# Kernel tuning notes

Hardware: AMD Instinct MI355X
Metric: run time of the kernel (lower is better)

The kernel has to match this reference:

```python
import jax, jax.numpy as jnp
from jax import lax
import numpy as np


def setup_inputs() -> dict:
    key = jax.random.key(0)
    ks = jax.random.split(key, 7)
    B, T, F, H, O = 4096, 256, 18, 64, 15
    s = 1.0 / np.sqrt(H)  # PyTorch uniform(-1/sqrt(H), 1/sqrt(H)) init scale
    return {
        "X": jax.random.normal(ks[0], (B, T, F), dtype=jnp.float32),
        "W_ih": jax.random.uniform(ks[1], (4 * H, F), jnp.float32, -s, s),
        "W_hh": jax.random.uniform(ks[2], (4 * H, H), jnp.float32, -s, s),
        "b_ih": jax.random.uniform(ks[3], (4 * H,), jnp.float32, -s, s),
        "b_hh": jax.random.uniform(ks[4], (4 * H,), jnp.float32, -s, s),
        "W_cls": jax.random.uniform(ks[5], (O, H), jnp.float32, -s, s),
        "b_cls": jax.random.uniform(ks[6], (O,), jnp.float32, -s, s),
    }


def _lstm_last_h(X, W_ih, W_hh, b_ih, b_hh):
    # X: [B, T, F]; PyTorch gate order in the 4H axis: i, f, g, o
    B = X.shape[0]
    H = W_hh.shape[1]
    # Input contribution for all timesteps at once: [B, T, 4H]
    xg = jnp.einsum("btf,gf->btg", X, W_ih) + b_ih + b_hh
    xg_t = jnp.swapaxes(xg, 0, 1)  # [T, B, 4H] for scan over time

    def step(carry, xg_step):
        h, c = carry
        gates = xg_step + h @ W_hh.T  # [B, 4H]
        i, f, g, o = jnp.split(gates, 4, axis=-1)
        i = jax.nn.sigmoid(i)
        f = jax.nn.sigmoid(f)
        g = jnp.tanh(g)
        o = jax.nn.sigmoid(o)
        c = f * c + i * g
        h = o * jnp.tanh(c)
        return (h, c), None

    h0 = jnp.zeros((B, H), dtype=X.dtype)
    c0 = jnp.zeros((B, H), dtype=X.dtype)
    (h, c), _ = lax.scan(step, (h0, c0), xg_t)
    return h  # last-timestep hidden state, [B, H]


def reference(X, W_ih, W_hh, b_ih, b_hh, W_cls, b_cls):
    h_last = _lstm_last_h(X, W_ih, W_hh, b_ih, b_hh)
    out = h_last @ W_cls.T + b_cls  # [B, n_outputs]
    return out
```

## Files before the change

kernel.cpp:

```cpp
#include <hip/hip_runtime.h>
#include <hip/hip_bf16.h>

typedef __attribute__((ext_vector_type(8))) __bf16 bf16x8;
typedef __attribute__((ext_vector_type(4))) float  f32x4;

#define T_SEQ 256
#define F_IN  18
#define HID   64
#define NB    16
#define NO    15

static __device__ __forceinline__ float rcp_fast(float x) {
    return __builtin_amdgcn_rcpf(x);
}
static __device__ __forceinline__ float sigm(float x) {
    return rcp_fast(1.0f + __expf(-x));
}
static __device__ __forceinline__ float tanh_fast(float x) {
    return 1.0f - 2.0f * rcp_fast(__expf(2.0f * x) + 1.0f);
}

#define BARRIER_LDS() asm volatile("s_waitcnt lgkmcnt(0)\n\ts_barrier" ::: "memory")

__global__ __launch_bounds__(1024, 4) void lstm_fused(
    const float* __restrict__ X,
    const float* __restrict__ Wih,
    const float* __restrict__ Whh,
    const float* __restrict__ bih,
    const float* __restrict__ bhh,
    const float* __restrict__ Wcls,
    const float* __restrict__ bcls,
    float* __restrict__ out)
{
    const int tid = threadIdx.x;
    const int l   = tid & 63;
    const int w   = tid >> 6;
    const int q   = l >> 4;
    const int bb  = l & 15;
    const int b0  = blockIdx.x * NB;

    __shared__ __align__(16) __bf16 hbuf[2][2][8][NB][8];
    __shared__ __align__(16) __bf16 xbuf[2][8][NB][8];
    __shared__ float h32[NB][HID];

    const int sb = (tid >> 3) & 15;
    const int sk = ((tid >> 7) << 3) | (tid & 7);
    int f_s, part_s;
    if (sk < 18)      { f_s = sk;      part_s = 0; }
    else if (sk < 36) { f_s = sk - 18; part_s = 0; }
    else if (sk < 54) { f_s = sk - 36; part_s = 1; }
    else              { f_s = 0;       part_s = 2; }
    const float* xsrc = X + ((long)(b0 + sb) * T_SEQ) * F_IN + f_s;
    __bf16* const xbase = &xbuf[0][0][0][0];

    {
        __bf16* hz = &hbuf[0][0][0][0][0];
        for (int i = tid; i < 2 * 8 * NB * 8; i += 1024) hz[i] = (__bf16)0.0f;
    }
    {
        const float v = (part_s == 2) ? 0.0f : xsrc[0];
        const __bf16 hi = (__bf16)v;
        xbase[tid] = (part_s == 1) ? (__bf16)(v - (float)hi) : hi;
    }
    float xq[4];
#pragma unroll
    for (int i = 0; i < 4; ++i)
        xq[i] = (part_s == 2) ? 0.0f : xsrc[(1 + i) * F_IN];

    bf16x8 whh_hi[2], whh_lo[2], wih[2];
    {
        const int prow = 16 * w + bb;
        const int jrow = (prow & 3) * 64 + (prow >> 2);
#pragma unroll
        for (int kk = 0; kk < 2; ++kk) {
            bf16x8 hi, lo, xa;
#pragma unroll
            for (int r = 0; r < 8; ++r) {
                const int k = 32 * kk + 8 * q + r;
                const float v = Whh[jrow * HID + k];
                const __bf16 vh = (__bf16)v;
                hi[r] = vh;
                lo[r] = (__bf16)(v - (float)vh);
                int f, part;
                if (k < 18)      { f = k;      part = 0; }
                else if (k < 36) { f = k - 18; part = 1; }
                else if (k < 54) { f = k - 36; part = 0; }
                else             { f = 0;      part = 2; }
                const float wv = (part == 2) ? 0.0f : Wih[jrow * F_IN + f];
                const __bf16 wh = (__bf16)wv;
                xa[r] = (part == 1) ? (__bf16)(wv - (float)wh) : wh;
            }
            whh_hi[kk] = hi;
            whh_lo[kk] = lo;
            wih[kk]    = xa;
        }
    }

    const int u_c = 4 * w + q;
    float bias4[4];
#pragma unroll
    for (int r = 0; r < 4; ++r) bias4[r] = bih[r * 64 + u_c] + bhh[r * 64 + u_c];

    __bf16* const hw_base = &hbuf[0][0][0][0][0] +
                            ((u_c >> 3) * 128 + bb * 8 + (u_c & 7));
    const __bf16* const hr_base = &hbuf[0][0][0][0][0] + 8 * (size_t)l;
    const __bf16* const xr_base = &xbuf[0][0][0][0] + 8 * (size_t)l;

    __syncthreads();

    float cst = 0.0f;

#pragma unroll 4
    for (int t = 0; t < T_SEQ; ++t) {
        const int cur = t & 1;
        const int nxt = cur ^ 1;
        const int s   = t & 3;

        const __bf16* hr = hr_base + cur * 2048;
        const __bf16* xr = xr_base + cur * 1024;
        const bf16x8 bx0 = *reinterpret_cast<const bf16x8*>(xr);
        const bf16x8 bx1 = *reinterpret_cast<const bf16x8*>(xr + 512);
        const bf16x8 bh0 = *reinterpret_cast<const bf16x8*>(hr);
        const bf16x8 bh1 = *reinterpret_cast<const bf16x8*>(hr + 512);
        const bf16x8 bl0 = *reinterpret_cast<const bf16x8*>(hr + 1024);
        const bf16x8 bl1 = *reinterpret_cast<const bf16x8*>(hr + 1536);

        {
            const float vs = xq[s];
            const __bf16 sh = (__bf16)vs;
            xbase[nxt * 1024 + tid] = (part_s == 1) ? (__bf16)(vs - (float)sh) : sh;
        }
        {
            const int tload = (t + 5 < T_SEQ) ? (t + 5) : (T_SEQ - 1);
            xq[s] = (part_s == 2) ? 0.0f : xsrc[tload * F_IN];
        }

        f32x4 acc_a = {bias4[0], bias4[1], bias4[2], bias4[3]};
        f32x4 acc_b = {0.0f, 0.0f, 0.0f, 0.0f};
        f32x4 acc_c = {0.0f, 0.0f, 0.0f, 0.0f};
        f32x4 acc_d = {0.0f, 0.0f, 0.0f, 0.0f};
        acc_a = __builtin_amdgcn_mfma_f32_16x16x32_bf16(wih[0],    bx0, acc_a, 0, 0, 0);
        acc_b = __builtin_amdgcn_mfma_f32_16x16x32_bf16(wih[1],    bx1, acc_b, 0, 0, 0);
        acc_c = __builtin_amdgcn_mfma_f32_16x16x32_bf16(whh_lo[0], bh0, acc_c, 0, 0, 0);
        acc_d = __builtin_amdgcn_mfma_f32_16x16x32_bf16(whh_lo[1], bh1, acc_d, 0, 0, 0);
        acc_a = __builtin_amdgcn_mfma_f32_16x16x32_bf16(whh_hi[0], bh0, acc_a, 0, 0, 0);
        acc_b = __builtin_amdgcn_mfma_f32_16x16x32_bf16(whh_hi[1], bh1, acc_b, 0, 0, 0);
        acc_c = __builtin_amdgcn_mfma_f32_16x16x32_bf16(whh_hi[0], bl0, acc_c, 0, 0, 0);
        acc_d = __builtin_amdgcn_mfma_f32_16x16x32_bf16(whh_hi[1], bl1, acc_d, 0, 0, 0);

        const f32x4 acc = (acc_a + acc_b) + (acc_c + acc_d);

        const float gi = sigm(acc[0]);
        const float gf = sigm(acc[1]);
        const float gg = tanh_fast(acc[2]);
        const float go = sigm(acc[3]);
        const float c  = gf * cst + gi * gg;
        cst = c;
        const float h  = go * tanh_fast(c);
        const __bf16 hh = (__bf16)h;
        const __bf16 hl = (__bf16)(h - (float)hh);
        __bf16* hw = hw_base + nxt * 2048;
        hw[0]    = hh;
        hw[1024] = hl;
        if (t == T_SEQ - 1) h32[bb][u_c] = h;

        BARRIER_LDS();
    }

    if (tid < NB * NO) {
        const int bo = tid / NO;
        const int o  = tid % NO;
        float ssum = bcls[o];
#pragma unroll 8
        for (int k = 0; k < HID; ++k)
            ssum += h32[bo][k] * Wcls[o * HID + k];
        out[(long)(b0 + bo) * NO + o] = ssum;
    }
}

extern "C" void kernel_launch(void* const* d_in, const int* in_sizes, int n_in,
                              void* d_out, int out_size, void* d_ws, size_t ws_size,
                              hipStream_t stream)
{
    const float* X    = (const float*)d_in[0];
    const float* Wih  = (const float*)d_in[1];
    const float* Whh  = (const float*)d_in[2];
    const float* bih  = (const float*)d_in[3];
    const float* bhh  = (const float*)d_in[4];
    const float* Wcls = (const float*)d_in[5];
    const float* bcls = (const float*)d_in[6];
    float* outp = (float*)d_out;

    dim3 grid(4096 / NB);
    dim3 block(1024);
    lstm_fused<<<grid, block, 0, stream>>>(X, Wih, Whh, bih, bhh, Wcls, bcls, outp);
}
```

Measured before the change: 282.8 us.

## Drop bf16 low part of hidden state, peel loop tail, add MFMA priority

Stores the recurrent hidden state as a single bf16 value instead of a hi/lo pair. This halves the h LDS buffer and reads, and cuts the per-step MFMA count from eight to six. The main loop is split into a 248-step body without the prefetch clamp or last-step check, plus a fully unrolled tail. s_setprio is raised around the MFMA and activation section. The cost is lower precision in the recurrence: h is rounded to bf16 with no compensation term, which may push the output error past tolerance over 256 steps.

```diff
diff --git a/kernel.cpp b/kernel.cpp
--- a/kernel.cpp
+++ b/kernel.cpp
@@ -39,7 +39,7 @@
     const int bb  = l & 15;
     const int b0  = blockIdx.x * NB;
 
-    __shared__ __align__(16) __bf16 hbuf[2][2][8][NB][8];
+    __shared__ __align__(16) __bf16 hbuf[2][8][NB][8];
     __shared__ __align__(16) __bf16 xbuf[2][8][NB][8];
     __shared__ float h32[NB][HID];
 
@@ -54,8 +54,8 @@
     __bf16* const xbase = &xbuf[0][0][0][0];
 
     {
-        __bf16* hz = &hbuf[0][0][0][0][0];
-        for (int i = tid; i < 2 * 8 * NB * 8; i += 1024) hz[i] = (__bf16)0.0f;
+        __bf16* hz = &hbuf[0][0][0][0];
+        for (int i = tid; i < 8 * NB * 8; i += 1024) hz[i] = (__bf16)0.0f;
     }
     {
         const float v = (part_s == 2) ? 0.0f : xsrc[0];
@@ -101,71 +101,69 @@
 #pragma unroll
     for (int r = 0; r < 4; ++r) bias4[r] = bih[r * 64 + u_c] + bhh[r * 64 + u_c];
 
-    __bf16* const hw_base = &hbuf[0][0][0][0][0] +
+    __bf16* const hw_base = &hbuf[0][0][0][0] +
                             ((u_c >> 3) * 128 + bb * 8 + (u_c & 7));
-    const __bf16* const hr_base = &hbuf[0][0][0][0][0] + 8 * (size_t)l;
+    const __bf16* const hr_base = &hbuf[0][0][0][0] + 8 * (size_t)l;
     const __bf16* const xr_base = &xbuf[0][0][0][0] + 8 * (size_t)l;
 
     __syncthreads();
 
     float cst = 0.0f;
 
+#define STEP(t_, PF, LAST)                                                          \
+    {                                                                               \
+        const int cur_ = (t_) & 1;                                                  \
+        const int nxt_ = cur_ ^ 1;                                                  \
+        const int s_   = (t_) & 3;                                                  \
+        const __bf16* hr = hr_base + cur_ * 1024;                                   \
+        const __bf16* xr = xr_base + cur_ * 1024;                                   \
+        const bf16x8 bx0 = *reinterpret_cast<const bf16x8*>(xr);                    \
+        const bf16x8 bx1 = *reinterpret_cast<const bf16x8*>(xr + 512);              \
+        const bf16x8 bh0 = *reinterpret_cast<const bf16x8*>(hr);                    \
+        const bf16x8 bh1 = *reinterpret_cast<const bf16x8*>(hr + 512);              \
+        {                                                                           \
+            const float vs = xq[s_];                                                \
+            const __bf16 sh = (__bf16)vs;                                           \
+            xbase[nxt_ * 1024 + tid] = (part_s == 1) ? (__bf16)(vs - (float)sh) : sh; \
+        }                                                                           \
+        {                                                                           \
+            const int tl_ = PF ? (((t_) + 5 < T_SEQ) ? (t_) + 5 : (T_SEQ - 1))      \
+                               : ((t_) + 5);                                        \
+            xq[s_] = (part_s == 2) ? 0.0f : xsrc[tl_ * F_IN];                       \
+        }                                                                           \
+        __builtin_amdgcn_s_setprio(1);                                              \
+        f32x4 acc_a = {bias4[0], bias4[1], bias4[2], bias4[3]};                     \
+        f32x4 acc_b = {0.0f, 0.0f, 0.0f, 0.0f};                                     \
+        f32x4 acc_c = {0.0f, 0.0f, 0.0f, 0.0f};                                     \
+        acc_a = __builtin_amdgcn_mfma_f32_16x16x32_bf16(wih[0],    bx0, acc_a, 0, 0, 0); \
+        acc_b = __builtin_amdgcn_mfma_f32_16x16x32_bf16(wih[1],    bx1, acc_b, 0, 0, 0); \
+        acc_c = __builtin_amdgcn_mfma_f32_16x16x32_bf16(whh_lo[0], bh0, acc_c, 0, 0, 0); \
+        acc_a = __builtin_amdgcn_mfma_f32_16x16x32_bf16(whh_hi[0], bh0, acc_a, 0, 0, 0); \
+        acc_b = __builtin_amdgcn_mfma_f32_16x16x32_bf16(whh_hi[1], bh1, acc_b, 0, 0, 0); \
+        acc_c = __builtin_amdgcn_mfma_f32_16x16x32_bf16(whh_lo[1], bh1, acc_c, 0, 0, 0); \
+        const f32x4 acc = (acc_a + acc_b) + acc_c;                                  \
+        const float gi = sigm(acc[0]);                                              \
+        const float gf = sigm(acc[1]);                                              \
+        const float gg = tanh_fast(acc[2]);                                         \
+        const float go = sigm(acc[3]);                                              \
+        const float c  = gf * cst + gi * gg;                                        \
+        cst = c;                                                                    \
+        const float h  = go * tanh_fast(c);                                         \
+        hw_base[nxt_ * 1024] = (__bf16)h;                                           \
+        __builtin_amdgcn_s_setprio(0);                                              \
+        if (LAST) h32[bb][u_c] = h;                                                 \
+        BARRIER_LDS();                                                              \
+    }
+
 #pragma unroll 4
-    for (int t = 0; t < T_SEQ; ++t) {
-        const int cur = t & 1;
-        const int nxt = cur ^ 1;
-        const int s   = t & 3;
-
-        const __bf16* hr = hr_base + cur * 2048;
-        const __bf16* xr = xr_base + cur * 1024;
-        const bf16x8 bx0 = *reinterpret_cast<const bf16x8*>(xr);
-        const bf16x8 bx1 = *reinterpret_cast<const bf16x8*>(xr + 512);
-        const bf16x8 bh0 = *reinterpret_cast<const bf16x8*>(hr);
-        const bf16x8 bh1 = *reinterpret_cast<const bf16x8*>(hr + 512);
-        const bf16x8 bl0 = *reinterpret_cast<const bf16x8*>(hr + 1024);
-        const bf16x8 bl1 = *reinterpret_cast<const bf16x8*>(hr + 1536);
-
-        {
-            const float vs = xq[s];
-            const __bf16 sh = (__bf16)vs;
-            xbase[nxt * 1024 + tid] = (part_s == 1) ? (__bf16)(vs - (float)sh) : sh;
-        }
-        {
-            const int tload = (t + 5 < T_SEQ) ? (t + 5) : (T_SEQ - 1);
-            xq[s] = (part_s == 2) ? 0.0f : xsrc[tload * F_IN];
-        }
-
-        f32x4 acc_a = {bias4[0], bias4[1], bias4[2], bias4[3]};
-        f32x4 acc_b = {0.0f, 0.0f, 0.0f, 0.0f};
-        f32x4 acc_c = {0.0f, 0.0f, 0.0f, 0.0f};
-        f32x4 acc_d = {0.0f, 0.0f, 0.0f, 0.0f};
-        acc_a = __builtin_amdgcn_mfma_f32_16x16x32_bf16(wih[0],    bx0, acc_a, 0, 0, 0);
-        acc_b = __builtin_amdgcn_mfma_f32_16x16x32_bf16(wih[1],    bx1, acc_b, 0, 0, 0);
-        acc_c = __builtin_amdgcn_mfma_f32_16x16x32_bf16(whh_lo[0], bh0, acc_c, 0, 0, 0);
-        acc_d = __builtin_amdgcn_mfma_f32_16x16x32_bf16(whh_lo[1], bh1, acc_d, 0, 0, 0);
-        acc_a = __builtin_amdgcn_mfma_f32_16x16x32_bf16(whh_hi[0], bh0, acc_a, 0, 0, 0);
-        acc_b = __builtin_amdgcn_mfma_f32_16x16x32_bf16(whh_hi[1], bh1, acc_b, 0, 0, 0);
-        acc_c = __builtin_amdgcn_mfma_f32_16x16x32_bf16(whh_hi[0], bl0, acc_c, 0, 0, 0);
-        acc_d = __builtin_amdgcn_mfma_f32_16x16x32_bf16(whh_hi[1], bl1, acc_d, 0, 0, 0);
-
-        const f32x4 acc = (acc_a + acc_b) + (acc_c + acc_d);
-
-        const float gi = sigm(acc[0]);
-        const float gf = sigm(acc[1]);
-        const float gg = tanh_fast(acc[2]);
-        const float go = sigm(acc[3]);
-        const float c  = gf * cst + gi * gg;
-        cst = c;
-        const float h  = go * tanh_fast(c);
-        const __bf16 hh = (__bf16)h;
-        const __bf16 hl = (__bf16)(h - (float)hh);
-        __bf16* hw = hw_base + nxt * 2048;
-        hw[0]    = hh;
-        hw[1024] = hl;
-        if (t == T_SEQ - 1) h32[bb][u_c] = h;
-
-        BARRIER_LDS();
+    for (int t = 0; t < 248; ++t) {
+        STEP(t, 0, 0)
     }
+#pragma unroll
+    for (int tt = 248; tt < T_SEQ; ++tt) {
+        STEP(tt, 1, (tt == T_SEQ - 1))
+    }
+#undef STEP
 
     if (tid < NB * NO) {
         const int bo = tid / NO;
```

Result: faster. 254.7 us (-9.9%).
